# Optimization experiments

Hardware: AMD Instinct MI355X
Metric: run time of the kernel (lower is better)

Reference implementation:

```python
import jax, jax.numpy as jnp
import numpy as np

D_MODEL = 1024
N_HEADS = 8
D_KEYS = D_MODEL // N_HEADS  # 128
D_LLM = 4096


def setup_inputs() -> dict:
    key = jax.random.key(0)
    ks = jax.random.split(key, 11)
    Bm, Lq, Vs = 8, 1024, 2048
    inner = D_KEYS * N_HEADS  # 1024
    s = 0.02
    return {
        "Q": jax.random.normal(ks[0], (Bm, Lq, D_MODEL), jnp.float32),
        "K_src": jax.random.normal(ks[1], (Vs, D_LLM), jnp.float32),
        "V_src": jax.random.normal(ks[2], (Vs, D_LLM), jnp.float32),
        "Wq": jax.random.normal(ks[3], (D_MODEL, inner), jnp.float32) * s,
        "bq": jnp.zeros((inner,), jnp.float32),
        "Wk": jax.random.normal(ks[4], (D_LLM, inner), jnp.float32) * s,
        "bk": jnp.zeros((inner,), jnp.float32),
        "Wv": jax.random.normal(ks[5], (D_LLM, inner), jnp.float32) * s,
        "bv": jnp.zeros((inner,), jnp.float32),
        "Wo": jax.random.normal(ks[6], (inner, D_LLM), jnp.float32) * s,
        "bo": jnp.zeros((D_LLM,), jnp.float32),
    }


def reference(Q, K_src, V_src, Wq, bq, Wk, bk, Wv, bv, Wo, bo):
    Bm, Lq, _ = Q.shape
    Vs, d_llm = K_src.shape
    H = N_HEADS
    Ek = d_llm // H  # NOTE: torch code scales by d_llm//H, not d_keys
    q = (Q @ Wq + bq).reshape(Bm, Lq, H, -1)           # [B,Lq,H,E]
    k = (K_src @ Wk + bk).reshape(Vs, H, -1)            # [S,H,E]
    v = (V_src @ Wv + bv).reshape(Vs, H, -1)            # [S,H,E]
    scale = 1.0 / jnp.sqrt(jnp.asarray(Ek, q.dtype))
    scores = jnp.einsum("blhe,she->bhls", q, k)         # [B,H,Lq,S]
    A = jax.nn.softmax(scale * scores, axis=-1)         # dropout = identity (eval)
    out = jnp.einsum("bhls,she->blhe", A, v)            # [B,Lq,H,E]
    out = out.reshape(Bm, Lq, -1)
    return out @ Wo + bo                                 # [B,Lq,d_llm]
```

## Files before the change

kernel.cpp:

```cpp
#include <hip/hip_runtime.h>
#include <hip/hip_bf16.h>


typedef __bf16 bf16x8 __attribute__((ext_vector_type(8)));
typedef float  f32x4  __attribute__((ext_vector_type(4)));

union V16 { uint4 u; bf16x8 v; };
__device__ __forceinline__ bf16x8 ld16v(const void* p) {
  V16 t; t.u = *(const uint4*)p; return t.v;
}
__device__ __forceinline__ uint4 pack8(float4 a, float4 b) {
  V16 t;
  t.v[0] = (__bf16)a.x; t.v[1] = (__bf16)a.y; t.v[2] = (__bf16)a.z; t.v[3] = (__bf16)a.w;
  t.v[4] = (__bf16)b.x; t.v[5] = (__bf16)b.y; t.v[6] = (__bf16)b.z; t.v[7] = (__bf16)b.w;
  return t.u;
}
__device__ __forceinline__ void dma16(const void* g, void* l) {
  __builtin_amdgcn_global_load_lds(
      (const __attribute__((address_space(1))) unsigned int*)g,
      (__attribute__((address_space(3))) unsigned int*)l, 16, 0, 0);
}
__device__ __forceinline__ float exp2_fast(float x) {
  float r;
  asm("v_exp_f32 %0, %1\n\ts_nop 1" : "=v"(r) : "v"(x));
  return r;
}
__device__ __forceinline__ int chunk_of(int row, int gc) {
  return row * 4 + (gc ^ ((row >> 1) & 3));
}

__global__ __launch_bounds__(256) void transpose_k(const float* __restrict__ W,
                                                   __bf16* __restrict__ Wt, int K, int N,
                                                   float scale) {
  __shared__ __bf16 t[32][33];
  int tx = threadIdx.x & 31, ty = threadIdx.x >> 5;
  int n0 = blockIdx.x * 32, k0 = blockIdx.y * 32;
#pragma unroll
  for (int r = 0; r < 32; r += 8)
    t[ty + r][tx] = (__bf16)(W[(size_t)(k0 + ty + r) * N + n0 + tx] * scale);
  __syncthreads();
#pragma unroll
  for (int r = 0; r < 32; r += 8) Wt[(size_t)(n0 + ty + r) * K + k0 + tx] = t[tx][ty + r];
}

template <typename AT, typename CT>
__device__ __forceinline__ void gemm_core(__bf16* As, __bf16* Bs,
                                          const AT* __restrict__ A,
                                          const __bf16* __restrict__ Bt,
                                          const float* __restrict__ bias,
                                          CT* __restrict__ C,
                                          int M, int N, int K, int lda, int trans,
                                          int m0, int n0, float bscale) {
  const int tid = threadIdx.x;
  const int lane = tid & 63, wave = tid >> 6;
  const int g = lane >> 4, l16 = lane & 15;
  const int wr = wave >> 1, wc = wave & 1;
  int aoff[4], boff[4];
#pragma unroll
  for (int mf = 0; mf < 4; mf++) aoff[mf] = chunk_of(wr * 64 + mf * 16 + l16, g) * 8;
#pragma unroll
  for (int nf = 0; nf < 4; nf++) boff[nf] = chunk_of(wc * 64 + nf * 16 + l16, g) * 8;

  f32x4 acc[4][4] = {};
  for (int k0 = 0; k0 < K; k0 += 32) {
    __syncthreads();
    if constexpr (sizeof(AT) == 2) {
#pragma unroll
      for (int rnd = 0; rnd < 2; rnd++) {
        int cstart = wave * 128 + rnd * 64;
        int p = cstart + lane;
        int row = p >> 2, gc = (p & 3) ^ ((row >> 1) & 3);
        dma16((const __bf16*)A + (size_t)(m0 + row) * lda + k0 + gc * 8,
              As + (size_t)cstart * 8);
      }
    } else {
#pragma unroll
      for (int i = 0; i < 2; i++) {
        int p = tid + i * 256;
        int row = p >> 2, gc = (p & 3) ^ ((row >> 1) & 3);
        const float* ap = (const float*)A + (size_t)(m0 + row) * lda + k0 + gc * 8;
        float4 f0 = *(const float4*)ap;
        float4 f1 = *(const float4*)(ap + 4);
        *(uint4*)(As + p * 8) = pack8(f0, f1);
      }
    }
#pragma unroll
    for (int rnd = 0; rnd < 2; rnd++) {
      int cstart = wave * 128 + rnd * 64;
      int p = cstart + lane;
      int row = p >> 2, gc = (p & 3) ^ ((row >> 1) & 3);
      dma16(Bt + (size_t)(n0 + row) * (size_t)K + k0 + gc * 8,
            Bs + (size_t)cstart * 8);
    }
    __syncthreads();
    bf16x8 af[4], bff[4];
#pragma unroll
    for (int mf = 0; mf < 4; mf++) af[mf]  = ld16v(As + aoff[mf]);
#pragma unroll
    for (int nf = 0; nf < 4; nf++) bff[nf] = ld16v(Bs + boff[nf]);
#pragma unroll
    for (int mf = 0; mf < 4; mf++)
#pragma unroll
      for (int nf = 0; nf < 4; nf++)
        acc[mf][nf] = __builtin_amdgcn_mfma_f32_16x16x32_bf16(af[mf], bff[nf], acc[mf][nf], 0, 0, 0);
  }
#pragma unroll
  for (int nf = 0; nf < 4; nf++) {
    int col = n0 + wc * 64 + nf * 16 + l16;
    float bv = bias[col] * bscale;
#pragma unroll
    for (int mf = 0; mf < 4; mf++) {
      int rowb = m0 + wr * 64 + mf * 16 + g * 4;
      if constexpr (sizeof(CT) == 2) {
        if (trans) {
          union { __bf16 h[4]; uint2 u; } pk;
#pragma unroll
          for (int r = 0; r < 4; r++) pk.h[r] = (__bf16)(acc[mf][nf][r] + bv);
          *(uint2*)&((__bf16*)C)[(size_t)col * M + rowb] = pk.u;
        } else {
#pragma unroll
          for (int r = 0; r < 4; r++)
            ((__bf16*)C)[(size_t)(rowb + r) * N + col] = (__bf16)(acc[mf][nf][r] + bv);
        }
      } else {
#pragma unroll
        for (int r = 0; r < 4; r++)
          ((float*)C)[(size_t)(rowb + r) * N + col] = acc[mf][nf][r] + bv;
      }
    }
  }
}

__global__ __launch_bounds__(256) void gemm_qkv(
    const float* __restrict__ Q,   const __bf16* __restrict__ WqT, const float* __restrict__ bq, __bf16* __restrict__ qb, float qscale,
    const float* __restrict__ Ksr, const __bf16* __restrict__ WkT, const float* __restrict__ bk, __bf16* __restrict__ kb,
    const float* __restrict__ Vsr, const __bf16* __restrict__ WvT, const float* __restrict__ bv, __bf16* __restrict__ vtb) {
  __shared__ __align__(16) __bf16 As[128 * 32];
  __shared__ __align__(16) __bf16 Bs[128 * 32];
  const int bid = blockIdx.x;
  if (bid < 512) {
    gemm_core<float, __bf16>(As, Bs, Q, WqT, bq, qb, 8192, 1024, 1024, 1024, 0,
                             (bid & 63) * 128, (bid >> 6) * 128, qscale);
  } else if (bid < 640) {
    const int b = bid - 512;
    gemm_core<float, __bf16>(As, Bs, Ksr, WkT, bk, kb, 2048, 1024, 4096, 4096, 0,
                             (b & 15) * 128, (b >> 4) * 128, 1.0f);
  } else {
    const int b = bid - 640;
    gemm_core<float, __bf16>(As, Bs, Vsr, WvT, bv, vtb, 2048, 1024, 4096, 4096, 1,
                             (b & 15) * 128, (b >> 4) * 128, 1.0f);
  }
}

__global__ __launch_bounds__(256) void gemm_b_f(const __bf16* __restrict__ A,
                                                const __bf16* __restrict__ Bt,
                                                const float* __restrict__ bias,
                                                float* __restrict__ C,
                                                int M, int N, int K, int lda, int trans) {
  __shared__ __align__(16) __bf16 As[128 * 32];
  __shared__ __align__(16) __bf16 Bs[128 * 32];
  gemm_core<__bf16, float>(As, Bs, A, Bt, bias, C, M, N, K, lda, trans,
                           blockIdx.x * 128, blockIdx.y * 128, 1.0f);
}

__global__ __launch_bounds__(512, 4) void attn_k(const __bf16* __restrict__ q,
                                                 const __bf16* __restrict__ k,
                                                 const __bf16* __restrict__ vt,
                                                 __bf16* __restrict__ o) {
  __shared__ __align__(16) __bf16 ks[2][64 * 128];
  __shared__ __align__(16) __bf16 vs[2][128 * 64];
  __shared__ __align__(16) __bf16 ps[128 * 64];
  const int tid = threadIdx.x, lane = tid & 63, wave = tid >> 6;
  const int g = lane >> 4, l16 = lane & 15;
  const int h = blockIdx.y, q0 = blockIdx.x * 128;

  const __bf16* kbase = k + (size_t)h * 128;
  const __bf16* vbase = vt + (size_t)(h * 128) * 2048;

  bf16x8 qf[4];
#pragma unroll
  for (int kk = 0; kk < 4; kk++)
    qf[kk] = ld16v(q + (size_t)(q0 + wave * 16 + l16) * 1024 + h * 128 + kk * 32 + g * 8);

  f32x4 accO[8] = {};
  float m_i[4], l_i[4];
#pragma unroll
  for (int r = 0; r < 4; r++) { m_i[r] = -1e30f; l_i[r] = 0.f; }

  {
#pragma unroll
    for (int i = 0; i < 2; i++) {
      int c = wave * 128 + i * 64 + lane;
      int row = c >> 4, gc = (c & 15) ^ (row & 7);
      dma16(kbase + (size_t)row * 1024 + gc * 8, &ks[0][(wave * 128 + i * 64) * 8]);
    }
#pragma unroll
    for (int i = 0; i < 2; i++) {
      int c = wave * 128 + i * 64 + lane;
      int row = c >> 3, cc = (c & 7) ^ (row & 7);
      dma16(vbase + (size_t)row * 2048 + cc * 8, &vs[0][(wave * 128 + i * 64) * 8]);
    }
  }

  for (int t = 0; t < 32; t++) {
    const int cur = t & 1;
    asm volatile("s_waitcnt lgkmcnt(0)" ::: "memory");
    __builtin_amdgcn_s_barrier();
    __builtin_amdgcn_sched_barrier(0);
    {
      const int sn = ((t + 1) & 31) * 64;
#pragma unroll
      for (int i = 0; i < 2; i++) {
        int c = wave * 128 + i * 64 + lane;
        int row = c >> 4, gc = (c & 15) ^ (row & 7);
        dma16(kbase + (size_t)(sn + row) * 1024 + gc * 8,
              &ks[cur ^ 1][(wave * 128 + i * 64) * 8]);
      }
#pragma unroll
      for (int i = 0; i < 2; i++) {
        int c = wave * 128 + i * 64 + lane;
        int row = c >> 3, cc = (c & 7) ^ (row & 7);
        dma16(vbase + (size_t)row * 2048 + sn + cc * 8,
              &vs[cur ^ 1][(wave * 128 + i * 64) * 8]);
      }
    }
    asm volatile("s_waitcnt vmcnt(4)" ::: "memory");
    __builtin_amdgcn_s_barrier();
    __builtin_amdgcn_sched_barrier(0);

    f32x4 sc[4] = {};
    __builtin_amdgcn_s_setprio(1);
#pragma unroll
    for (int kk = 0; kk < 4; kk++) {
      bf16x8 kf[4];
#pragma unroll
      for (int nf = 0; nf < 4; nf++) {
        int row = nf * 16 + l16;
        kf[nf] = ld16v(&ks[cur][(row * 16 + ((kk * 4 + g) ^ (row & 7))) * 8]);
      }
#pragma unroll
      for (int nf = 0; nf < 4; nf++)
        sc[nf] = __builtin_amdgcn_mfma_f32_16x16x32_bf16(qf[kk], kf[nf], sc[nf], 0, 0, 0);
    }
    __builtin_amdgcn_s_setprio(0);

#pragma unroll
    for (int r = 0; r < 4; r++) {
      float mx = fmaxf(fmaxf(sc[0][r], sc[1][r]), fmaxf(sc[2][r], sc[3][r]));
#pragma unroll
      for (int off = 1; off < 16; off <<= 1) mx = fmaxf(mx, __shfl_xor(mx, off));
      float mn = fmaxf(m_i[r], mx);
      float alpha = exp2_fast(m_i[r] - mn);
      float rs = 0.f;
#pragma unroll
      for (int nf = 0; nf < 4; nf++) {
        float p = exp2_fast(sc[nf][r] - mn);
        sc[nf][r] = p;
        rs += p;
      }
#pragma unroll
      for (int off = 1; off < 16; off <<= 1) rs += __shfl_xor(rs, off);
      m_i[r] = mn;
      l_i[r] = l_i[r] * alpha + rs;
#pragma unroll
      for (int ef = 0; ef < 8; ef++) accO[ef][r] *= alpha;
    }

#pragma unroll
    for (int nf = 0; nf < 4; nf++)
#pragma unroll
      for (int r = 0; r < 4; r++) {
        int prow = wave * 16 + g * 4 + r;
        int cc = nf * 2 + (l16 >> 3);
        ps[(prow * 8 + (cc ^ (prow & 7))) * 8 + (l16 & 7)] = (__bf16)sc[nf][r];
      }

    __builtin_amdgcn_s_setprio(1);
#pragma unroll
    for (int kk = 0; kk < 2; kk++) {
      int prow = wave * 16 + l16;
      bf16x8 pf = ld16v(&ps[(prow * 8 + ((kk * 4 + g) ^ (prow & 7))) * 8]);
#pragma unroll
      for (int ef = 0; ef < 8; ef++) {
        int vrow = ef * 16 + l16;
        bf16x8 vf = ld16v(&vs[cur][(vrow * 8 + ((kk * 4 + g) ^ (vrow & 7))) * 8]);
        accO[ef] = __builtin_amdgcn_mfma_f32_16x16x32_bf16(pf, vf, accO[ef], 0, 0, 0);
      }
    }
    __builtin_amdgcn_s_setprio(0);
  }

  float inv[4];
#pragma unroll
  for (int r = 0; r < 4; r++) inv[r] = 1.0f / l_i[r];
#pragma unroll
  for (int ef = 0; ef < 8; ef++)
#pragma unroll
    for (int r = 0; r < 4; r++) {
      int row = q0 + wave * 16 + g * 4 + r;
      o[(size_t)row * 1024 + h * 128 + ef * 16 + l16] = (__bf16)(accO[ef][r] * inv[r]);
    }
}

extern "C" void kernel_launch(void* const* d_in, const int* in_sizes, int n_in,
                              void* d_out, int out_size, void* d_ws, size_t ws_size,
                              hipStream_t stream) {
  const float* Q   = (const float*)d_in[0];
  const float* Ksr = (const float*)d_in[1];
  const float* Vsr = (const float*)d_in[2];
  const float* Wq  = (const float*)d_in[3];
  const float* bq  = (const float*)d_in[4];
  const float* Wk  = (const float*)d_in[5];
  const float* bk  = (const float*)d_in[6];
  const float* Wv  = (const float*)d_in[7];
  const float* bv  = (const float*)d_in[8];
  const float* Wo  = (const float*)d_in[9];
  const float* bo  = (const float*)d_in[10];
  __bf16* ws = (__bf16*)d_ws;
  const size_t MB = 1024 * 1024;
  __bf16* qb  = ws;
  __bf16* kb  = ws + 8  * MB;
  __bf16* vtb = ws + 10 * MB;
  __bf16* at  = ws + 12 * MB;
  __bf16* WqT = ws + 20 * MB;
  __bf16* WkT = ws + 21 * MB;
  __bf16* WvT = ws + 25 * MB;
  __bf16* WoT = ws + 29 * MB;

  const float qscale = 0.044194173824159216f * 1.4426950408889634f;

  transpose_k<<<dim3(32, 32),  256, 0, stream>>>(Wq, WqT, 1024, 1024, qscale);
  transpose_k<<<dim3(32, 128), 256, 0, stream>>>(Wk, WkT, 4096, 1024, 1.0f);
  transpose_k<<<dim3(32, 128), 256, 0, stream>>>(Wv, WvT, 4096, 1024, 1.0f);
  transpose_k<<<dim3(128, 32), 256, 0, stream>>>(Wo, WoT, 1024, 4096, 1.0f);

  gemm_qkv<<<dim3(768), 256, 0, stream>>>(Q, WqT, bq, qb, qscale,
                                          Ksr, WkT, bk, kb,
                                          Vsr, WvT, bv, vtb);
  attn_k<<<dim3(64, 8), 512, 0, stream>>>(qb, kb, vtb, at);
  gemm_b_f<<<dim3(64, 32), 256, 0, stream>>>(at, WoT, bo, (float*)d_out, 8192, 4096, 1024, 1024, 0);
}
```

Before: 659.8 us.

## Double-buffer GEMM shared-memory tiles to overlap global loads with MFMA

Restructures the shared GEMM core into a software pipeline. The next K-tile is prefetched into an alternate LDS buffer through global_load_lds for bf16 operands, or into registers for fp32 A, while MFMAs run on the current tile. Explicit waitcnt and barrier placement replaces the two __syncthreads per iteration, and s_setprio is raised around the MFMA block. This aims to hide global memory latency in the projection GEMMs, at the cost of extra LDS and registers and fragile manual vmcnt counting.

Result: no change. 662.4 us (+0.4%).

```diff
diff --git a/kernel.cpp b/kernel.cpp
--- a/kernel.cpp
+++ b/kernel.cpp
@@ -44,7 +44,8 @@
 }
 
 template <typename AT, typename CT>
-__device__ __forceinline__ void gemm_core(__bf16* As, __bf16* Bs,
+__device__ __forceinline__ void gemm_core(__bf16* As0, __bf16* As1,
+                                          __bf16* Bs0, __bf16* Bs1,
                                           const AT* __restrict__ A,
                                           const __bf16* __restrict__ Bt,
                                           const float* __restrict__ bias,
@@ -61,48 +62,98 @@
 #pragma unroll
   for (int nf = 0; nf < 4; nf++) boff[nf] = chunk_of(wc * 64 + nf * 16 + l16, g) * 8;
 
+  const int cA = wave * 128 + lane;
+  const int p0 = tid, p1 = tid + 256;
+
   f32x4 acc[4][4] = {};
-  for (int k0 = 0; k0 < K; k0 += 32) {
-    __syncthreads();
+  float4 a0l, a0h, a1l, a1h;
+
+  if constexpr (sizeof(AT) == 2) {
+#pragma unroll
+    for (int rnd = 0; rnd < 2; rnd++) {
+      int c = cA + rnd * 64;
+      int row = c >> 2, gc = (c & 3) ^ ((row >> 1) & 3);
+      dma16((const __bf16*)A + (size_t)(m0 + row) * lda + gc * 8,
+            As0 + (wave * 128 + rnd * 64) * 8);
+    }
+  } else {
+    { int row = p0 >> 2, gc = (p0 & 3) ^ ((row >> 1) & 3);
+      const float* ap = (const float*)A + (size_t)(m0 + row) * lda + gc * 8;
+      a0l = *(const float4*)ap; a0h = *(const float4*)(ap + 4); }
+    { int row = p1 >> 2, gc = (p1 & 3) ^ ((row >> 1) & 3);
+      const float* ap = (const float*)A + (size_t)(m0 + row) * lda + gc * 8;
+      a1l = *(const float4*)ap; a1h = *(const float4*)(ap + 4); }
+  }
+#pragma unroll
+  for (int rnd = 0; rnd < 2; rnd++) {
+    int c = cA + rnd * 64;
+    int row = c >> 2, gc = (c & 3) ^ ((row >> 1) & 3);
+    dma16(Bt + (size_t)(n0 + row) * (size_t)K + gc * 8,
+          Bs0 + (wave * 128 + rnd * 64) * 8);
+  }
+
+  for (int k0 = 0, t = 0; k0 < K; k0 += 32, t++) {
+    __bf16* Ac = (t & 1) ? As1 : As0;
+    __bf16* An = (t & 1) ? As0 : As1;
+    __bf16* Bc = (t & 1) ? Bs1 : Bs0;
+    __bf16* Bn = (t & 1) ? Bs0 : Bs1;
+    if constexpr (sizeof(AT) != 2) Ac = As0;
+    const int kn = (k0 + 32 < K) ? k0 + 32 : 0;
+    asm volatile("s_waitcnt lgkmcnt(0)" ::: "memory");
+    __builtin_amdgcn_s_barrier();
+    __builtin_amdgcn_sched_barrier(0);
     if constexpr (sizeof(AT) == 2) {
 #pragma unroll
       for (int rnd = 0; rnd < 2; rnd++) {
-        int cstart = wave * 128 + rnd * 64;
-        int p = cstart + lane;
-        int row = p >> 2, gc = (p & 3) ^ ((row >> 1) & 3);
-        dma16((const __bf16*)A + (size_t)(m0 + row) * lda + k0 + gc * 8,
-              As + (size_t)cstart * 8);
-      }
+        int c = cA + rnd * 64;
+        int row = c >> 2, gc = (c & 3) ^ ((row >> 1) & 3);
+        dma16((const __bf16*)A + (size_t)(m0 + row) * lda + kn + gc * 8,
+              An + (wave * 128 + rnd * 64) * 8);
+      }
+#pragma unroll
+      for (int rnd = 0; rnd < 2; rnd++) {
+        int c = cA + rnd * 64;
+        int row = c >> 2, gc = (c & 3) ^ ((row >> 1) & 3);
+        dma16(Bt + (size_t)(n0 + row) * (size_t)K + kn + gc * 8,
+              Bn + (wave * 128 + rnd * 64) * 8);
+      }
+      __builtin_amdgcn_sched_barrier(0);
+      asm volatile("s_waitcnt vmcnt(4)" ::: "memory");
     } else {
-#pragma unroll
-      for (int i = 0; i < 2; i++) {
-        int p = tid + i * 256;
-        int row = p >> 2, gc = (p & 3) ^ ((row >> 1) & 3);
-        const float* ap = (const float*)A + (size_t)(m0 + row) * lda + k0 + gc * 8;
-        float4 f0 = *(const float4*)ap;
-        float4 f1 = *(const float4*)(ap + 4);
-        *(uint4*)(As + p * 8) = pack8(f0, f1);
-      }
-    }
-#pragma unroll
-    for (int rnd = 0; rnd < 2; rnd++) {
-      int cstart = wave * 128 + rnd * 64;
-      int p = cstart + lane;
-      int row = p >> 2, gc = (p & 3) ^ ((row >> 1) & 3);
-      dma16(Bt + (size_t)(n0 + row) * (size_t)K + k0 + gc * 8,
-            Bs + (size_t)cstart * 8);
-    }
-    __syncthreads();
+      *(uint4*)(Ac + p0 * 8) = pack8(a0l, a0h);
+      *(uint4*)(Ac + p1 * 8) = pack8(a1l, a1h);
+      __builtin_amdgcn_sched_barrier(0);
+      { int row = p0 >> 2, gc = (p0 & 3) ^ ((row >> 1) & 3);
+        const float* ap = (const float*)A + (size_t)(m0 + row) * lda + kn + gc * 8;
+        a0l = *(const float4*)ap; a0h = *(const float4*)(ap + 4); }
+      { int row = p1 >> 2, gc = (p1 & 3) ^ ((row >> 1) & 3);
+        const float* ap = (const float*)A + (size_t)(m0 + row) * lda + kn + gc * 8;
+        a1l = *(const float4*)ap; a1h = *(const float4*)(ap + 4); }
+#pragma unroll
+      for (int rnd = 0; rnd < 2; rnd++) {
+        int c = cA + rnd * 64;
+        int row = c >> 2, gc = (c & 3) ^ ((row >> 1) & 3);
+        dma16(Bt + (size_t)(n0 + row) * (size_t)K + kn + gc * 8,
+              Bn + (wave * 128 + rnd * 64) * 8);
+      }
+      __builtin_amdgcn_sched_barrier(0);
+      asm volatile("s_waitcnt vmcnt(6) lgkmcnt(0)" ::: "memory");
+    }
+    __builtin_amdgcn_s_barrier();
+    __builtin_amdgcn_sched_barrier(0);
+
     bf16x8 af[4], bff[4];
 #pragma unroll
-    for (int mf = 0; mf < 4; mf++) af[mf]  = ld16v(As + aoff[mf]);
-#pragma unroll
-    for (int nf = 0; nf < 4; nf++) bff[nf] = ld16v(Bs + boff[nf]);
+    for (int mf = 0; mf < 4; mf++) af[mf]  = ld16v(Ac + aoff[mf]);
+#pragma unroll
+    for (int nf = 0; nf < 4; nf++) bff[nf] = ld16v(Bc + boff[nf]);
+    __builtin_amdgcn_s_setprio(1);
 #pragma unroll
     for (int mf = 0; mf < 4; mf++)
 #pragma unroll
       for (int nf = 0; nf < 4; nf++)
         acc[mf][nf] = __builtin_amdgcn_mfma_f32_16x16x32_bf16(af[mf], bff[nf], acc[mf][nf], 0, 0, 0);
+    __builtin_amdgcn_s_setprio(0);
   }
 #pragma unroll
   for (int nf = 0; nf < 4; nf++) {
@@ -136,18 +187,18 @@
     const float* __restrict__ Ksr, const __bf16* __restrict__ WkT, const float* __restrict__ bk, __bf16* __restrict__ kb,
     const float* __restrict__ Vsr, const __bf16* __restrict__ WvT, const float* __restrict__ bv, __bf16* __restrict__ vtb) {
   __shared__ __align__(16) __bf16 As[128 * 32];
-  __shared__ __align__(16) __bf16 Bs[128 * 32];
+  __shared__ __align__(16) __bf16 Bs[2][128 * 32];
   const int bid = blockIdx.x;
   if (bid < 512) {
-    gemm_core<float, __bf16>(As, Bs, Q, WqT, bq, qb, 8192, 1024, 1024, 1024, 0,
+    gemm_core<float, __bf16>(As, As, Bs[0], Bs[1], Q, WqT, bq, qb, 8192, 1024, 1024, 1024, 0,
                              (bid & 63) * 128, (bid >> 6) * 128, qscale);
   } else if (bid < 640) {
     const int b = bid - 512;
-    gemm_core<float, __bf16>(As, Bs, Ksr, WkT, bk, kb, 2048, 1024, 4096, 4096, 0,
+    gemm_core<float, __bf16>(As, As, Bs[0], Bs[1], Ksr, WkT, bk, kb, 2048, 1024, 4096, 4096, 0,
                              (b & 15) * 128, (b >> 4) * 128, 1.0f);
   } else {
     const int b = bid - 640;
-    gemm_core<float, __bf16>(As, Bs, Vsr, WvT, bv, vtb, 2048, 1024, 4096, 4096, 1,
+    gemm_core<float, __bf16>(As, As, Bs[0], Bs[1], Vsr, WvT, bv, vtb, 2048, 1024, 4096, 4096, 1,
                              (b & 15) * 128, (b >> 4) * 128, 1.0f);
   }
 }
@@ -157,9 +208,9 @@
                                                 const float* __restrict__ bias,
                                                 float* __restrict__ C,
                                                 int M, int N, int K, int lda, int trans) {
-  __shared__ __align__(16) __bf16 As[128 * 32];
-  __shared__ __align__(16) __bf16 Bs[128 * 32];
-  gemm_core<__bf16, float>(As, Bs, A, Bt, bias, C, M, N, K, lda, trans,
+  __shared__ __align__(16) __bf16 As[2][128 * 32];
+  __shared__ __align__(16) __bf16 Bs[2][128 * 32];
+  gemm_core<__bf16, float>(As[0], As[1], Bs[0], Bs[1], A, Bt, bias, C, M, N, K, lda, trans,
                            blockIdx.x * 128, blockIdx.y * 128, 1.0f);
 }
 
```

## Split-K the K/V projections and rebalance Q tiles across blocks

Applied to the files above, without the earlier changes.

The long-K (4096) K and V projection tiles are split into two K-halves, each written as a bf16 partial, and a new finalize kernel sums them. The Q projection blocks now each compute two adjacent N tiles, so all 768 blocks carry roughly equal work instead of a few long K/V blocks trailing. Attention output is written in place over the q buffer, which frees workspace for the partials. The cost is an extra kernel launch, extra partial-buffer traffic and one more bf16 rounding of K and V.

New measurement: 636.6 us. -3.5%, faster.

```diff
diff --git a/kernel.cpp b/kernel.cpp
--- a/kernel.cpp
+++ b/kernel.cpp
@@ -49,7 +49,7 @@
                                           const __bf16* __restrict__ Bt,
                                           const float* __restrict__ bias,
                                           CT* __restrict__ C,
-                                          int M, int N, int K, int lda, int trans,
+                                          int M, int N, int K, int lda, int ldb, int trans,
                                           int m0, int n0, float bscale) {
   const int tid = threadIdx.x;
   const int lane = tid & 63, wave = tid >> 6;
@@ -89,7 +89,7 @@
       int cstart = wave * 128 + rnd * 64;
       int p = cstart + lane;
       int row = p >> 2, gc = (p & 3) ^ ((row >> 1) & 3);
-      dma16(Bt + (size_t)(n0 + row) * (size_t)K + k0 + gc * 8,
+      dma16(Bt + (size_t)(n0 + row) * (size_t)ldb + k0 + gc * 8,
             Bs + (size_t)cstart * 8);
     }
     __syncthreads();
@@ -133,23 +133,49 @@
 
 __global__ __launch_bounds__(256) void gemm_qkv(
     const float* __restrict__ Q,   const __bf16* __restrict__ WqT, const float* __restrict__ bq, __bf16* __restrict__ qb, float qscale,
-    const float* __restrict__ Ksr, const __bf16* __restrict__ WkT, const float* __restrict__ bk, __bf16* __restrict__ kb,
-    const float* __restrict__ Vsr, const __bf16* __restrict__ WvT, const float* __restrict__ bv, __bf16* __restrict__ vtb) {
+    const float* __restrict__ Ksr, const __bf16* __restrict__ WkT, const float* __restrict__ bk, __bf16* __restrict__ kp0, __bf16* __restrict__ kp1,
+    const float* __restrict__ Vsr, const __bf16* __restrict__ WvT, const float* __restrict__ bv, __bf16* __restrict__ vp0, __bf16* __restrict__ vp1) {
   __shared__ __align__(16) __bf16 As[128 * 32];
   __shared__ __align__(16) __bf16 Bs[128 * 32];
   const int bid = blockIdx.x;
-  if (bid < 512) {
-    gemm_core<float, __bf16>(As, Bs, Q, WqT, bq, qb, 8192, 1024, 1024, 1024, 0,
-                             (bid & 63) * 128, (bid >> 6) * 128, qscale);
-  } else if (bid < 640) {
+  if (bid < 256) {
+    const int m0 = (bid & 63) * 128, n0 = (bid >> 6) * 256;
+    gemm_core<float, __bf16>(As, Bs, Q, WqT, bq, qb, 8192, 1024, 1024, 1024, 1024, 0,
+                             m0, n0, qscale);
+    gemm_core<float, __bf16>(As, Bs, Q, WqT, bq, qb, 8192, 1024, 1024, 1024, 1024, 0,
+                             m0, n0 + 128, qscale);
+  } else if (bid < 512) {
+    const int b = bid - 256;
+    const int grp = b >> 7, bb = b & 127;
+    __bf16* dst = grp ? kp1 : kp0;
+    gemm_core<float, __bf16>(As, Bs, Ksr + grp * 2048, WkT + grp * 2048, bk, dst,
+                             2048, 1024, 2048, 4096, 4096, 0,
+                             (bb & 15) * 128, (bb >> 4) * 128, grp == 0 ? 1.0f : 0.0f);
+  } else {
     const int b = bid - 512;
-    gemm_core<float, __bf16>(As, Bs, Ksr, WkT, bk, kb, 2048, 1024, 4096, 4096, 0,
-                             (b & 15) * 128, (b >> 4) * 128, 1.0f);
-  } else {
-    const int b = bid - 640;
-    gemm_core<float, __bf16>(As, Bs, Vsr, WvT, bv, vtb, 2048, 1024, 4096, 4096, 1,
-                             (b & 15) * 128, (b >> 4) * 128, 1.0f);
-  }
+    const int grp = b >> 7, bb = b & 127;
+    __bf16* dst = grp ? vp1 : vp0;
+    gemm_core<float, __bf16>(As, Bs, Vsr + grp * 2048, WvT + grp * 2048, bv, dst,
+                             2048, 1024, 2048, 4096, 4096, 1,
+                             (bb & 15) * 128, (bb >> 4) * 128, grp == 0 ? 1.0f : 0.0f);
+  }
+}
+
+__global__ __launch_bounds__(256) void finalize2(
+    const __bf16* __restrict__ kp0, const __bf16* __restrict__ kp1, __bf16* __restrict__ kb,
+    const __bf16* __restrict__ vp0, const __bf16* __restrict__ vp1, __bf16* __restrict__ vtb) {
+  int i = blockIdx.x * 256 + threadIdx.x;
+  const __bf16 *a, *b;
+  __bf16* d;
+  int j;
+  if (i < 262144) { a = kp0; b = kp1; d = kb;  j = i; }
+  else            { a = vp0; b = vp1; d = vtb; j = i - 262144; }
+  bf16x8 x = ld16v(a + (size_t)j * 8);
+  bf16x8 y = ld16v(b + (size_t)j * 8);
+  V16 o;
+#pragma unroll
+  for (int t = 0; t < 8; t++) o.v[t] = (__bf16)((float)x[t] + (float)y[t]);
+  *(uint4*)(d + (size_t)j * 8) = o.u;
 }
 
 __global__ __launch_bounds__(256) void gemm_b_f(const __bf16* __restrict__ A,
@@ -159,14 +185,14 @@
                                                 int M, int N, int K, int lda, int trans) {
   __shared__ __align__(16) __bf16 As[128 * 32];
   __shared__ __align__(16) __bf16 Bs[128 * 32];
-  gemm_core<__bf16, float>(As, Bs, A, Bt, bias, C, M, N, K, lda, trans,
+  gemm_core<__bf16, float>(As, Bs, A, Bt, bias, C, M, N, K, lda, K, trans,
                            blockIdx.x * 128, blockIdx.y * 128, 1.0f);
 }
 
-__global__ __launch_bounds__(512, 4) void attn_k(const __bf16* __restrict__ q,
+__global__ __launch_bounds__(512, 4) void attn_k(const __bf16* q,
                                                  const __bf16* __restrict__ k,
                                                  const __bf16* __restrict__ vt,
-                                                 __bf16* __restrict__ o) {
+                                                 __bf16* o) {
   __shared__ __align__(16) __bf16 ks[2][64 * 128];
   __shared__ __align__(16) __bf16 vs[2][128 * 64];
   __shared__ __align__(16) __bf16 ps[128 * 64];
@@ -321,7 +347,10 @@
   __bf16* qb  = ws;
   __bf16* kb  = ws + 8  * MB;
   __bf16* vtb = ws + 10 * MB;
-  __bf16* at  = ws + 12 * MB;
+  __bf16* kp0 = ws + 12 * MB;
+  __bf16* kp1 = ws + 14 * MB;
+  __bf16* vp0 = ws + 16 * MB;
+  __bf16* vp1 = ws + 18 * MB;
   __bf16* WqT = ws + 20 * MB;
   __bf16* WkT = ws + 21 * MB;
   __bf16* WvT = ws + 25 * MB;
@@ -335,8 +364,9 @@
   transpose_k<<<dim3(128, 32), 256, 0, stream>>>(Wo, WoT, 1024, 4096, 1.0f);
 
   gemm_qkv<<<dim3(768), 256, 0, stream>>>(Q, WqT, bq, qb, qscale,
-                                          Ksr, WkT, bk, kb,
-                                          Vsr, WvT, bv, vtb);
-  attn_k<<<dim3(64, 8), 512, 0, stream>>>(qb, kb, vtb, at);
-  gemm_b_f<<<dim3(64, 32), 256, 0, stream>>>(at, WoT, bo, (float*)d_out, 8192, 4096, 1024, 1024, 0);
-}
+                                          Ksr, WkT, bk, kp0, kp1,
+                                          Vsr, WvT, bv, vp0, vp1);
+  finalize2<<<dim3(2048), 256, 0, stream>>>(kp0, kp1, kb, vp0, vp1, vtb);
+  attn_k<<<dim3(64, 8), 512, 0, stream>>>(qb, kb, vtb, qb);
+  gemm_b_f<<<dim3(64, 32), 256, 0, stream>>>(qb, WoT, bo, (float*)d_out, 8192, 4096, 1024, 1024, 0);
+}
```
